# Performance work log

Hardware: AMD Instinct MI355X
Metric: run time of the kernel (lower is better)

Reference implementation:

```python
import jax, jax.numpy as jnp
import numpy as np

TOKENS = 16384
HID = 2048


def _per_channel_scale(w, b):
    # scale per output channel, as in _apply_per_channel_scaling
    s = jnp.clip(jnp.max(jnp.abs(w), axis=1), 1e-6, None)  # [out]
    return w / s[:, None], b / s, s[None, :]  # scaled weight, scaled bias, scale row-vector


def setup_inputs() -> dict:
    key = jax.random.key(0)
    k = jax.random.split(key, 5)
    x = jax.random.normal(k[0], (TOKENS, HID), dtype=jnp.float32)
    w1_raw = jax.random.normal(k[1], (2 * HID, HID), dtype=jnp.float32) * 0.02
    b1_raw = jax.random.normal(k[2], (2 * HID,), dtype=jnp.float32) * 0.02
    w2_raw = jax.random.normal(k[3], (HID, 2 * HID), dtype=jnp.float32) * 0.02
    b2_raw = jax.random.normal(k[4], (HID,), dtype=jnp.float32) * 0.02
    w1, b1, s1 = _per_channel_scale(w1_raw, b1_raw)
    w2, b2, s2 = _per_channel_scale(w2_raw, b2_raw)
    return {"x": x, "w1": w1, "b1": b1, "s1": s1, "w2": w2, "b2": b2, "s2": s2}


def reference(x, w1, b1, s1, w2, b2, s2):
    # fc1 (scaled weights) -> per-channel dequant scale -> exact GELU -> fc2 -> scale
    h = (x @ w1.T + b1) * s1            # [T, 2H]
    h = jax.nn.gelu(h, approximate=False)
    y = (h @ w2.T + b2) * s2            # [T, H]
    return y
```

## Files before the change

kernel.cpp:

```cpp
#include <hip/hip_runtime.h>
#include <math.h>

typedef __attribute__((ext_vector_type(8))) short short8;
typedef __attribute__((ext_vector_type(4))) float f32x4;

#define GLOBAL_AS __attribute__((address_space(1)))
#define LDS_AS __attribute__((address_space(3)))

__device__ __forceinline__ unsigned short f2bf(float f) {
  union { float f; unsigned u; } v; v.f = f;
  unsigned r = v.u + 0x7fffu + ((v.u >> 16) & 1u);
  return (unsigned short)(r >> 16);
}

__global__ void cvt_f32_to_bf16(const float* __restrict__ in,
                                unsigned short* __restrict__ out, int n4) {
  int i = blockIdx.x * blockDim.x + threadIdx.x;
  if (i < n4) {
    const float4 v = ((const float4*)in)[i];
    ushort4 o;
    o.x = f2bf(v.x); o.y = f2bf(v.y); o.z = f2bf(v.z); o.w = f2bf(v.w);
    ((ushort4*)out)[i] = o;
  }
}

template <int EPI>
__global__ __launch_bounds__(512, 2) void gemm256_8ph(
    const unsigned short* __restrict__ A, const unsigned short* __restrict__ B,
    const float* __restrict__ bias, const float* __restrict__ scale,
    void* __restrict__ Cout, int M, int N, int K) {
  constexpr int BM = 256, BN = 256;
  __shared__ __attribute__((aligned(16))) unsigned short ldsA[32768];
  __shared__ __attribute__((aligned(16))) unsigned short ldsB[32768];

  const int NT = K >> 6;
  const int nTn = N / BN;
  const int bid = blockIdx.x;
  const int cpx = gridDim.x >> 3;
  const int wg = (bid & 7) * cpx + (bid >> 3);
  const int tm = wg / nTn, tn = wg % nTn;

  const int tid = threadIdx.x;
  const int w = tid >> 6, l = tid & 63;
  const int wr = w >> 2, wc = w & 3;
  const int lr = l & 15, g = l >> 4;

  const unsigned short* Ag = A + (size_t)tm * BM * K;
  const unsigned short* Bg = B + (size_t)tn * BN * K;

  size_t gs0, gs1;
  {
    int p0 = tid * 16, p1 = tid * 16 + 8192;
    int sp0 = p0 ^ (((p0 >> 7) & 7) << 4);
    int sp1 = p1 ^ (((p1 >> 7) & 7) << 4);
    gs0 = (size_t)(sp0 >> 6) * K + ((sp0 & 63) >> 1);
    gs1 = (size_t)(sp1 >> 6) * K + ((sp1 & 63) >> 1);
  }
  const unsigned short* pA0 = Ag + gs0; const unsigned short* pA1 = Ag + gs1;
  const unsigned short* pB0 = Bg + gs0; const unsigned short* pB1 = Bg + gs1;
  const int ldsWaveOff = w * 512;

#define STAGE_A(tau, ks, SLOT)                                                   \
  if ((tau) < NT) {                                                              \
    const size_t ko_ = ((size_t)(tau) << 6) + ((ks) << 5);                       \
    __builtin_amdgcn_global_load_lds((const GLOBAL_AS void*)(pA0 + ko_),         \
        (LDS_AS void*)(ldsA + (SLOT)*8192 + ldsWaveOff), 16, 0, 0);              \
    __builtin_amdgcn_global_load_lds((const GLOBAL_AS void*)(pA1 + ko_),         \
        (LDS_AS void*)(ldsA + (SLOT)*8192 + 4096 + ldsWaveOff), 16, 0, 0);       \
  }
#define STAGE_B(tau, ks, SLOT)                                                   \
  if ((tau) < NT) {                                                              \
    const size_t ko_ = ((size_t)(tau) << 6) + ((ks) << 5);                       \
    __builtin_amdgcn_global_load_lds((const GLOBAL_AS void*)(pB0 + ko_),         \
        (LDS_AS void*)(ldsB + (SLOT)*8192 + ldsWaveOff), 16, 0, 0);              \
    __builtin_amdgcn_global_load_lds((const GLOBAL_AS void*)(pB1 + ko_),         \
        (LDS_AS void*)(ldsB + (SLOT)*8192 + 4096 + ldsWaveOff), 16, 0, 0);       \
  }

  int ab = ((wr * 128 + lr) << 6) + (g << 4);
  int aoff = ab ^ (((ab >> 7) & 7) << 4);
  int bb = ((wc * 64 + lr) << 6) + (g << 4);
  int boff = bb ^ (((bb >> 7) & 7) << 4);
  const char* ldsAb = (const char*)ldsA + aoff;
  const char* ldsBb = (const char*)ldsB + boff;
#define LDA8(S, H, m) (*(const short8*)(ldsAb + (S)*16384 + (H)*4096 + (m)*1024))
#define LDB8(S, n)    (*(const short8*)(ldsBb + (S)*16384 + (n)*1024))

  f32x4 acc[8][4] = {};
  short8 a[4], b[4];

#define OPEN_MFMA(ROW0)                                                          \
  __builtin_amdgcn_s_barrier();                                                  \
  asm volatile("s_waitcnt lgkmcnt(0)" ::: "memory");                             \
  __builtin_amdgcn_s_setprio(1);                                                 \
  _Pragma("unroll") for (int m = 0; m < 4; ++m)                                  \
  _Pragma("unroll") for (int n = 0; n < 4; ++n)                                  \
    acc[(ROW0) + m][n] = __builtin_amdgcn_mfma_f32_16x16x32_bf16(                \
        a[m], b[n], acc[(ROW0) + m][n], 0, 0, 0);                                \
  __builtin_amdgcn_s_setprio(0);

  STAGE_A(0, 0, 0) STAGE_B(0, 0, 0)
  STAGE_A(0, 1, 1) STAGE_B(0, 1, 1)
  STAGE_A(1, 0, 2) STAGE_B(1, 0, 2)
  asm volatile("s_waitcnt vmcnt(4)" ::: "memory");
  __builtin_amdgcn_s_barrier();

  for (int kt = 0; kt < NT; kt += 2) {
    const bool full = (kt + 2 < NT);
#pragma unroll
    for (int m = 0; m < 4; ++m) a[m] = LDA8(0, 0, m);
#pragma unroll
    for (int n = 0; n < 4; ++n) b[n] = LDB8(0, n);
    STAGE_A(kt + 1, 1, 3)
    OPEN_MFMA(0)
    __builtin_amdgcn_s_barrier();
#pragma unroll
    for (int m = 0; m < 4; ++m) a[m] = LDA8(0, 1, m);
    STAGE_B(kt + 1, 1, 3)
    OPEN_MFMA(4)
    asm volatile("s_waitcnt vmcnt(4)" ::: "memory");
    __builtin_amdgcn_s_barrier();
#pragma unroll
    for (int m = 0; m < 4; ++m) a[m] = LDA8(1, 0, m);
#pragma unroll
    for (int n = 0; n < 4; ++n) b[n] = LDB8(1, n);
    STAGE_A(kt + 2, 0, 0)
    OPEN_MFMA(0)
    __builtin_amdgcn_s_barrier();
#pragma unroll
    for (int m = 0; m < 4; ++m) a[m] = LDA8(1, 1, m);
    STAGE_B(kt + 2, 0, 0)
    OPEN_MFMA(4)
    if (full) { asm volatile("s_waitcnt vmcnt(4)" ::: "memory"); }
    else      { asm volatile("s_waitcnt vmcnt(2)" ::: "memory"); }
    __builtin_amdgcn_s_barrier();
#pragma unroll
    for (int m = 0; m < 4; ++m) a[m] = LDA8(2, 0, m);
#pragma unroll
    for (int n = 0; n < 4; ++n) b[n] = LDB8(2, n);
    STAGE_A(kt + 2, 1, 1)
    OPEN_MFMA(0)
    __builtin_amdgcn_s_barrier();
#pragma unroll
    for (int m = 0; m < 4; ++m) a[m] = LDA8(2, 1, m);
    STAGE_B(kt + 2, 1, 1)
    OPEN_MFMA(4)
    if (full) { asm volatile("s_waitcnt vmcnt(4)" ::: "memory"); }
    else      { asm volatile("s_waitcnt vmcnt(0)" ::: "memory"); }
    __builtin_amdgcn_s_barrier();
#pragma unroll
    for (int m = 0; m < 4; ++m) a[m] = LDA8(3, 0, m);
#pragma unroll
    for (int n = 0; n < 4; ++n) b[n] = LDB8(3, n);
    STAGE_A(kt + 3, 0, 2)
    OPEN_MFMA(0)
    __builtin_amdgcn_s_barrier();
#pragma unroll
    for (int m = 0; m < 4; ++m) a[m] = LDA8(3, 1, m);
    STAGE_B(kt + 3, 0, 2)
    OPEN_MFMA(4)
    if (full) { asm volatile("s_waitcnt vmcnt(4)" ::: "memory"); }
    else      { asm volatile("s_waitcnt vmcnt(0)" ::: "memory"); }
    __builtin_amdgcn_s_barrier();
  }

  const int orow = tm * BM + wr * 128;
  const int ocol = tn * BN + wc * 64;
  const int rsub = g * 4;
#pragma unroll
  for (int n = 0; n < 4; ++n) {
    const int gn = ocol + n * 16 + lr;
    const float bv = bias[gn];
    const float sv = scale[gn];
#pragma unroll
    for (int m = 0; m < 8; ++m) {
#pragma unroll
      for (int j = 0; j < 4; ++j) {
        const int gm = orow + m * 16 + rsub + j;
        float v = (acc[m][n][j] + bv) * sv;
        if (EPI == 0) {
          const float gl = 0.5f * v * (1.0f + erff(v * 0.70710678118654752440f));
          ((unsigned short*)Cout)[(size_t)gm * N + gn] = f2bf(gl);
        } else {
          ((float*)Cout)[(size_t)gm * N + gn] = v;
        }
      }
    }
  }
#undef STAGE_A
#undef STAGE_B
#undef LDA8
#undef LDB8
#undef OPEN_MFMA
}

extern "C" void kernel_launch(void* const* d_in, const int* in_sizes, int n_in,
                              void* d_out, int out_size, void* d_ws, size_t ws_size,
                              hipStream_t stream) {
  const int T = 16384, H = 2048, H2 = 4096;
  const float* x  = (const float*)d_in[0];
  const float* w1 = (const float*)d_in[1];
  const float* b1 = (const float*)d_in[2];
  const float* s1 = (const float*)d_in[3];
  const float* w2 = (const float*)d_in[4];
  const float* b2 = (const float*)d_in[5];
  const float* s2 = (const float*)d_in[6];

  unsigned short* xb  = (unsigned short*)d_ws;
  unsigned short* w1b = xb  + (size_t)T  * H;
  unsigned short* w2b = w1b + (size_t)H2 * H;
  unsigned short* hb  = w2b + (size_t)H  * H2;

  int n4 = T * H / 4;
  cvt_f32_to_bf16<<<(n4 + 255) / 256, 256, 0, stream>>>(x, xb, n4);
  n4 = H2 * H / 4;
  cvt_f32_to_bf16<<<(n4 + 255) / 256, 256, 0, stream>>>(w1, w1b, n4);
  cvt_f32_to_bf16<<<(n4 + 255) / 256, 256, 0, stream>>>(w2, w2b, n4);

  gemm256_8ph<0><<<(T / 256) * (H2 / 256), 512, 0, stream>>>(
      xb, w1b, b1, s1, (void*)hb, T, H2, H);
  gemm256_8ph<1><<<(T / 256) * (H / 256), 512, 0, stream>>>(
      hb, w2b, b2, s2, d_out, T, H, H2);
}
```

Baseline: 851.9 us.

## Restructure GEMM LDS layout to full-K64 rows with double-buffered A and triple-slot B

Replaces the split ldsA/ldsB arrays of 32-wide K slices with one LDS buffer holding 64-wide K rows (128-byte rows, XOR swizzle). A is double-buffered per 64-K tile, and B rotates through three half-tile slots. The main loop is rewritten as a two-tile macro with fewer, larger global-to-LDS transfers and a new vmcnt wait schedule. The aim is fewer waits per K step and more contiguous global reads, at the risk of new LDS bank conflicts or hazards in the slot rotation.

```diff
diff --git a/kernel.cpp b/kernel.cpp
--- a/kernel.cpp
+++ b/kernel.cpp
@@ -25,13 +25,12 @@
 }
 
 template <int EPI>
-__global__ __launch_bounds__(512, 2) void gemm256_8ph(
+__global__ __launch_bounds__(512, 2) void gemm256_v5(
     const unsigned short* __restrict__ A, const unsigned short* __restrict__ B,
     const float* __restrict__ bias, const float* __restrict__ scale,
     void* __restrict__ Cout, int M, int N, int K) {
   constexpr int BM = 256, BN = 256;
-  __shared__ __attribute__((aligned(16))) unsigned short ldsA[32768];
-  __shared__ __attribute__((aligned(16))) unsigned short ldsB[32768];
+  __shared__ __attribute__((aligned(16))) unsigned short ldsAll[65536];
 
   const int NT = K >> 6;
   const int nTn = N / BN;
@@ -48,43 +47,42 @@
   const unsigned short* Ag = A + (size_t)tm * BM * K;
   const unsigned short* Bg = B + (size_t)tn * BN * K;
 
-  size_t gs0, gs1;
-  {
-    int p0 = tid * 16, p1 = tid * 16 + 8192;
-    int sp0 = p0 ^ (((p0 >> 7) & 7) << 4);
-    int sp1 = p1 ^ (((p1 >> 7) & 7) << 4);
-    gs0 = (size_t)(sp0 >> 6) * K + ((sp0 & 63) >> 1);
-    gs1 = (size_t)(sp1 >> 6) * K + ((sp1 & 63) >> 1);
+  const int rowt = tid >> 3;
+  const int colsh = ((((tid & 7) * 16) ^ ((rowt & 7) << 4)) >> 1);
+  const size_t segK = (size_t)64 * K;
+  const unsigned short* pA0g = Ag + (size_t)rowt * K + colsh;
+  const unsigned short* pA1g = Ag + ((size_t)128 + rowt) * K + colsh;
+  const unsigned short* pB0g = Bg + (size_t)rowt * K + colsh;
+  const unsigned short* pB1g = Bg + ((size_t)128 + rowt) * K + colsh;
+
+  char* const LB = (char*)ldsAll;
+  const int wl = w * 1024;
+
+#define STAGE_AH(tau, h, DB)                                                     \
+  if ((tau) < NT) {                                                              \
+    const unsigned short* q_ = ((h) ? pA1g : pA0g) + (size_t)(tau) * 64;         \
+    __builtin_amdgcn_global_load_lds((const GLOBAL_AS void*)q_,                  \
+        (LDS_AS void*)(LB + (DB) * 32768 + (h) * 16384 + wl), 16, 0, 0);         \
+    __builtin_amdgcn_global_load_lds((const GLOBAL_AS void*)(q_ + segK),         \
+        (LDS_AS void*)(LB + (DB) * 32768 + (h) * 16384 + 8192 + wl), 16, 0, 0);  \
   }
-  const unsigned short* pA0 = Ag + gs0; const unsigned short* pA1 = Ag + gs1;
-  const unsigned short* pB0 = Bg + gs0; const unsigned short* pB1 = Bg + gs1;
-  const int ldsWaveOff = w * 512;
-
-#define STAGE_A(tau, ks, SLOT)                                                   \
+#define STAGE_BH(tau, h, SLOT)                                                   \
   if ((tau) < NT) {                                                              \
-    const size_t ko_ = ((size_t)(tau) << 6) + ((ks) << 5);                       \
-    __builtin_amdgcn_global_load_lds((const GLOBAL_AS void*)(pA0 + ko_),         \
-        (LDS_AS void*)(ldsA + (SLOT)*8192 + ldsWaveOff), 16, 0, 0);              \
-    __builtin_amdgcn_global_load_lds((const GLOBAL_AS void*)(pA1 + ko_),         \
-        (LDS_AS void*)(ldsA + (SLOT)*8192 + 4096 + ldsWaveOff), 16, 0, 0);       \
-  }
-#define STAGE_B(tau, ks, SLOT)                                                   \
-  if ((tau) < NT) {                                                              \
-    const size_t ko_ = ((size_t)(tau) << 6) + ((ks) << 5);                       \
-    __builtin_amdgcn_global_load_lds((const GLOBAL_AS void*)(pB0 + ko_),         \
-        (LDS_AS void*)(ldsB + (SLOT)*8192 + ldsWaveOff), 16, 0, 0);              \
-    __builtin_amdgcn_global_load_lds((const GLOBAL_AS void*)(pB1 + ko_),         \
-        (LDS_AS void*)(ldsB + (SLOT)*8192 + 4096 + ldsWaveOff), 16, 0, 0);       \
+    const unsigned short* q_ = ((h) ? pB1g : pB0g) + (size_t)(tau) * 64;         \
+    __builtin_amdgcn_global_load_lds((const GLOBAL_AS void*)q_,                  \
+        (LDS_AS void*)(LB + 65536 + (SLOT) * 16384 + wl), 16, 0, 0);             \
+    __builtin_amdgcn_global_load_lds((const GLOBAL_AS void*)(q_ + segK),         \
+        (LDS_AS void*)(LB + 65536 + (SLOT) * 16384 + 8192 + wl), 16, 0, 0);      \
   }
 
-  int ab = ((wr * 128 + lr) << 6) + (g << 4);
-  int aoff = ab ^ (((ab >> 7) & 7) << 4);
-  int bb = ((wc * 64 + lr) << 6) + (g << 4);
-  int boff = bb ^ (((bb >> 7) & 7) << 4);
-  const char* ldsAb = (const char*)ldsA + aoff;
-  const char* ldsBb = (const char*)ldsB + boff;
-#define LDA8(S, H, m) (*(const short8*)(ldsAb + (S)*16384 + (H)*4096 + (m)*1024))
-#define LDB8(S, n)    (*(const short8*)(ldsBb + (S)*16384 + (n)*1024))
+  const int sig0 = (g * 16) ^ ((lr & 7) << 4);
+  const int sig1 = (64 + g * 16) ^ ((lr & 7) << 4);
+  const char* Ab0 = LB + wr * 16384 + lr * 128 + sig0;
+  const char* Ab1 = LB + wr * 16384 + lr * 128 + sig1;
+  const char* Bb0 = LB + 65536 + (wc >> 1) * 16384 + (wc & 1) * 8192 + lr * 128 + sig0;
+  const char* Bb1 = LB + 65536 + (wc >> 1) * 16384 + (wc & 1) * 8192 + lr * 128 + sig1;
+#define LDA8(KS, DB, m) (*(const short8*)(((KS) ? Ab1 : Ab0) + (DB) * 32768 + (m) * 2048))
+#define LDB8(KS, TP, n) (*(const short8*)(((KS) ? Bb1 : Bb0) + (TP) * 32768 + (n) * 2048))
 
   f32x4 acc[8][4] = {};
   short8 a[4], b[4];
@@ -99,69 +97,44 @@
         a[m], b[n], acc[(ROW0) + m][n], 0, 0, 0);                                \
   __builtin_amdgcn_s_setprio(0);
 
-  STAGE_A(0, 0, 0) STAGE_B(0, 0, 0)
-  STAGE_A(0, 1, 1) STAGE_B(0, 1, 1)
-  STAGE_A(1, 0, 2) STAGE_B(1, 0, 2)
-  asm volatile("s_waitcnt vmcnt(4)" ::: "memory");
+#define TILE_BODY(T_, DB_, TP_, SBHI_, SBLO_, FULL_)                             \
+  {                     \
+    _Pragma("unroll") for (int m = 0; m < 4; ++m) a[m] = LDA8(0, DB_, m);        \
+    _Pragma("unroll") for (int n = 0; n < 4; ++n) b[n] = LDB8(0, TP_, n);        \
+    STAGE_AH((T_) + 1, 0, (DB_) ^ 1)                                             \
+    STAGE_AH((T_) + 1, 1, (DB_) ^ 1)                                             \
+    STAGE_BH((T_) + 1, 1, SBHI_)                                                 \
+    OPEN_MFMA(0)                                                                 \
+    __builtin_amdgcn_s_barrier();                                                \
+                                        \
+    _Pragma("unroll") for (int m = 0; m < 4; ++m) a[m] = LDA8(0, DB_, 4 + m);    \
+    OPEN_MFMA(4)                                                                 \
+    __builtin_amdgcn_s_barrier();                                                \
+                                                 \
+    _Pragma("unroll") for (int m = 0; m < 4; ++m) a[m] = LDA8(1, DB_, m);        \
+    _Pragma("unroll") for (int n = 0; n < 4; ++n) b[n] = LDB8(1, TP_, n);        \
+    OPEN_MFMA(0)                                                                 \
+    __builtin_amdgcn_s_barrier();                                                \
+      \
+    _Pragma("unroll") for (int m = 0; m < 4; ++m) a[m] = LDA8(1, DB_, 4 + m);    \
+    STAGE_BH((T_) + 2, 0, SBLO_)                                                 \
+    OPEN_MFMA(4)                                                                 \
+    if (FULL_) { asm volatile("s_waitcnt vmcnt(2)" ::: "memory"); }              \
+    else       { asm volatile("s_waitcnt vmcnt(0)" ::: "memory"); }              \
+    __builtin_amdgcn_s_barrier();                                                \
+  }
+
+  STAGE_AH(0, 0, 0)
+  STAGE_AH(0, 1, 0)
+  STAGE_BH(0, 0, 0)
+  STAGE_BH(0, 1, 1)
+  STAGE_BH(1, 0, 2)
+  asm volatile("s_waitcnt vmcnt(2)" ::: "memory");
   __builtin_amdgcn_s_barrier();
 
   for (int kt = 0; kt < NT; kt += 2) {
-    const bool full = (kt + 2 < NT);
-#pragma unroll
-    for (int m = 0; m < 4; ++m) a[m] = LDA8(0, 0, m);
-#pragma unroll
-    for (int n = 0; n < 4; ++n) b[n] = LDB8(0, n);
-    STAGE_A(kt + 1, 1, 3)
-    OPEN_MFMA(0)
-    __builtin_amdgcn_s_barrier();
-#pragma unroll
-    for (int m = 0; m < 4; ++m) a[m] = LDA8(0, 1, m);
-    STAGE_B(kt + 1, 1, 3)
-    OPEN_MFMA(4)
-    asm volatile("s_waitcnt vmcnt(4)" ::: "memory");
-    __builtin_amdgcn_s_barrier();
-#pragma unroll
-    for (int m = 0; m < 4; ++m) a[m] = LDA8(1, 0, m);
-#pragma unroll
-    for (int n = 0; n < 4; ++n) b[n] = LDB8(1, n);
-    STAGE_A(kt + 2, 0, 0)
-    OPEN_MFMA(0)
-    __builtin_amdgcn_s_barrier();
-#pragma unroll
-    for (int m = 0; m < 4; ++m) a[m] = LDA8(1, 1, m);
-    STAGE_B(kt + 2, 0, 0)
-    OPEN_MFMA(4)
-    if (full) { asm volatile("s_waitcnt vmcnt(4)" ::: "memory"); }
-    else      { asm volatile("s_waitcnt vmcnt(2)" ::: "memory"); }
-    __builtin_amdgcn_s_barrier();
-#pragma unroll
-    for (int m = 0; m < 4; ++m) a[m] = LDA8(2, 0, m);
-#pragma unroll
-    for (int n = 0; n < 4; ++n) b[n] = LDB8(2, n);
-    STAGE_A(kt + 2, 1, 1)
-    OPEN_MFMA(0)
-    __builtin_amdgcn_s_barrier();
-#pragma unroll
-    for (int m = 0; m < 4; ++m) a[m] = LDA8(2, 1, m);
-    STAGE_B(kt + 2, 1, 1)
-    OPEN_MFMA(4)
-    if (full) { asm volatile("s_waitcnt vmcnt(4)" ::: "memory"); }
-    else      { asm volatile("s_waitcnt vmcnt(0)" ::: "memory"); }
-    __builtin_amdgcn_s_barrier();
-#pragma unroll
-    for (int m = 0; m < 4; ++m) a[m] = LDA8(3, 0, m);
-#pragma unroll
-    for (int n = 0; n < 4; ++n) b[n] = LDB8(3, n);
-    STAGE_A(kt + 3, 0, 2)
-    OPEN_MFMA(0)
-    __builtin_amdgcn_s_barrier();
-#pragma unroll
-    for (int m = 0; m < 4; ++m) a[m] = LDA8(3, 1, m);
-    STAGE_B(kt + 3, 0, 2)
-    OPEN_MFMA(4)
-    if (full) { asm volatile("s_waitcnt vmcnt(4)" ::: "memory"); }
-    else      { asm volatile("s_waitcnt vmcnt(0)" ::: "memory"); }
-    __builtin_amdgcn_s_barrier();
+    TILE_BODY(kt, 0, 0, 3, 0, (kt + 2 < NT))
+    TILE_BODY(kt + 1, 1, 1, 1, 2, (kt + 3 < NT))
   }
 
   const int orow = tm * BM + wr * 128;
@@ -187,11 +160,12 @@
       }
     }
   }
-#undef STAGE_A
-#undef STAGE_B
+#undef STAGE_AH
+#undef STAGE_BH
 #undef LDA8
 #undef LDB8
 #undef OPEN_MFMA
+#undef TILE_BODY
 }
 
 extern "C" void kernel_launch(void* const* d_in, const int* in_sizes, int n_in,
@@ -217,8 +191,8 @@
   cvt_f32_to_bf16<<<(n4 + 255) / 256, 256, 0, stream>>>(w1, w1b, n4);
   cvt_f32_to_bf16<<<(n4 + 255) / 256, 256, 0, stream>>>(w2, w2b, n4);
 
-  gemm256_8ph<0><<<(T / 256) * (H2 / 256), 512, 0, stream>>>(
+  gemm256_v5<0><<<(T / 256) * (H2 / 256), 512, 0, stream>>>(
       xb, w1b, b1, s1, (void*)hb, T, H2, H);
-  gemm256_8ph<1><<<(T / 256) * (H / 256), 512, 0, stream>>>(
+  gemm256_v5<1><<<(T / 256) * (H / 256), 512, 0, stream>>>(
       hb, w2b, b2, s2, d_out, T, H, H2);
 }
```

Result: faster. 812.7 us (-4.6%).
